# Kernel optimization log

Hardware: AMD Instinct MI355X
Metric: run time of the kernel (lower is better)

Reference implementation:

```python
import jax, jax.numpy as jnp
import numpy as np

N = 100000   # nodes
R = 4        # relations
E = 160000   # edges per relation
DIN = 128
DOUT = 128


def setup_inputs() -> dict:
    key = jax.random.key(0)
    k = jax.random.split(key, 5)
    x = jax.random.normal(k[0], (N, DIN), dtype=jnp.float32)
    src = jax.random.randint(k[1], (R, E), 0, N, dtype=jnp.int32)
    dst = jax.random.randint(k[2], (R, E), 0, N, dtype=jnp.int32)
    # per-relation weights (Linear.weight.T in the original), xavier-ish scale
    W = jax.random.normal(k[3], (R, DIN, DOUT), dtype=jnp.float32) / np.sqrt(DIN)
    Wl = jax.random.normal(k[4], (DIN, DOUT), dtype=jnp.float32) / np.sqrt(DIN)
    b = jnp.zeros((DOUT,), dtype=jnp.float32)
    return {"x": x, "W": W, "Wl": Wl, "b": b, "src": src, "dst": dst}


def reference(x, W, Wl, b, src, dst):
    # DGL GraphConv(norm='right', in==out): aggregate messages first, then matmul.
    def per_rel(s, d):
        agg = jax.ops.segment_sum(x[s], d, num_segments=N)          # [N, DIN]
        deg = jax.ops.segment_sum(jnp.ones(s.shape, x.dtype), d, num_segments=N)
        return agg / jnp.clip(deg, 1.0)[:, None]                     # right norm

    aggs = jax.vmap(per_rel)(src, dst)            # [R, N, DIN]
    h = jnp.einsum('rnd,rde->ne', aggs, W)        # per-relation GEMM + sum over relations
    h = h + x @ Wl + b                            # self-loop Linear with bias
    return jax.nn.relu(h)                         # activation; dropout p=0.0 is identity
```

## Files before the change

### kernel.cpp

```cpp
#include <hip/hip_runtime.h>

#define DIN 128
#define DOUT 128

typedef float f4 __attribute__((ext_vector_type(4)));
typedef float f32x4 __attribute__((ext_vector_type(4)));
typedef short bf16x8 __attribute__((ext_vector_type(8)));
typedef unsigned short u16x8 __attribute__((ext_vector_type(8)));
typedef unsigned short u16x4 __attribute__((ext_vector_type(4)));

__device__ inline unsigned short f2bf(float f) {
    unsigned u = __float_as_uint(f);
    u += 0x7FFFu + ((u >> 16) & 1u);
    return (unsigned short)(u >> 16);
}

__global__ void prep_w(const float* __restrict__ W, const float* __restrict__ Wl,
                       unsigned short* __restrict__ Wt, int total) {
    int id = blockIdx.x * 256 + threadIdx.x;
    if (id >= total) return;
    int m    = id >> 14;
    int rem  = id & 16383;
    int din  = rem >> 7;
    int dout = rem & 127;
    float v = (m < 4) ? W[(m << 14) + din * DOUT + dout] : Wl[din * DOUT + dout];
    Wt[(m << 14) + dout * DIN + din] = f2bf(v);
}

__global__ void prep_x(const float* __restrict__ x, unsigned short* __restrict__ xbf,
                       int total) {
    int tid = blockIdx.x * 256 + threadIdx.x;
    if (tid >= total) return;
    const float* xr = x + (long long)tid * 8;
    f4 lo = *(const f4*)xr;
    f4 hi = *(const f4*)(xr + 4);
    u16x8 p;
    p[0] = f2bf(lo[0]); p[1] = f2bf(lo[1]); p[2] = f2bf(lo[2]); p[3] = f2bf(lo[3]);
    p[4] = f2bf(hi[0]); p[5] = f2bf(hi[1]); p[6] = f2bf(hi[2]); p[7] = f2bf(hi[3]);
    *(u16x8*)&xbf[(long long)tid * 8] = p;
}

__global__ void deg_count(const int* __restrict__ dst, int* __restrict__ cnt,
                          int E, int N, int total) {
    int i = blockIdx.x * 256 + threadIdx.x;
    if (i >= total) return;
    int r = i / E;
    atomicAdd(&cnt[r * N + dst[i]], 1);
}

__global__ void scan1(const int* __restrict__ cnt, int* __restrict__ off,
                      int* __restrict__ part, int M) {
    __shared__ int sd[256];
    const int t = threadIdx.x, b = blockIdx.x;
    const int base = b * 2048 + t * 8;
    int v[8]; int tsum = 0;
    #pragma unroll
    for (int i = 0; i < 8; i++) { int g = base + i; v[i] = (g < M) ? cnt[g] : 0; tsum += v[i]; }
    sd[t] = tsum; __syncthreads();
    for (int d = 1; d < 256; d <<= 1) {
        int val = 0;
        if (t >= d) val = sd[t - d];
        __syncthreads();
        if (t >= d) sd[t] += val;
        __syncthreads();
    }
    int run = sd[t] - tsum;
    if (t == 255) part[b] = sd[255];
    #pragma unroll
    for (int i = 0; i < 8; i++) { int g = base + i; if (g < M) off[g] = run; run += v[i]; }
}

__global__ void scan2(int* __restrict__ part, int nb, int* __restrict__ offM) {
    __shared__ int sd[256];
    const int t = threadIdx.x;
    int v = (t < nb) ? part[t] : 0;
    sd[t] = v; __syncthreads();
    for (int d = 1; d < 256; d <<= 1) {
        int val = 0;
        if (t >= d) val = sd[t - d];
        __syncthreads();
        if (t >= d) sd[t] += val;
        __syncthreads();
    }
    if (t < nb) part[t] = sd[t] - v;
    if (t == 255) *offM = sd[255];
}

__global__ void scan3(int* __restrict__ off, const int* __restrict__ part, int M) {
    const int add = part[blockIdx.x];
    const int base = blockIdx.x * 2048 + threadIdx.x;
    #pragma unroll
    for (int i = 0; i < 8; i++) { int g = base + i * 256; if (g < M) off[g] += add; }
}

__global__ void fill_csr(const int* __restrict__ src, const int* __restrict__ dst,
                         const int* __restrict__ off, int* __restrict__ cnt,
                         int* __restrict__ csr, int E, int N, int total) {
    int i = blockIdx.x * 256 + threadIdx.x;
    if (i >= total) return;
    int r = i / E;
    int idx = r * N + dst[i];
    int pos = atomicAdd(&cnt[idx], -1) - 1;
    csr[off[idx] + pos] = src[i];
}

__global__ __launch_bounds__(256)
void gather_bf(const unsigned short* __restrict__ xbf, const int* __restrict__ off,
               const int* __restrict__ csr, unsigned short* __restrict__ agg,
               int N, int total) {
    int tid = blockIdx.x * 256 + threadIdx.x;
    if (tid >= total) return;
    const int c  = tid & 15;
    const int nn = tid >> 4;
    const int n  = nn % N;
    const int rr = nn / N;

    const int idx = rr * N + n;
    const int s0 = off[idx];
    const int s1 = off[idx + 1];

    float acc[8];
    #pragma unroll
    for (int i = 0; i < 8; i++) acc[i] = 0.0f;

    for (int e = s0; e < s1; e++) {
        const int s = csr[e];
        u16x8 v = *(const u16x8*)&xbf[(long long)s * DIN + c * 8];
        #pragma unroll
        for (int i = 0; i < 8; i++)
            acc[i] += __uint_as_float(((unsigned)v[i]) << 16);
    }
    const float sc = 1.0f / fmaxf((float)(s1 - s0), 1.0f);
    u16x8 p;
    #pragma unroll
    for (int i = 0; i < 8; i++) p[i] = f2bf(acc[i] * sc);
    *(u16x8*)&agg[((long long)rr * N + n) * DIN + c * 8] = p;
}

__global__ __launch_bounds__(256)
void gather_f32(const float* __restrict__ x, const int* __restrict__ off,
                const int* __restrict__ csr, unsigned short* __restrict__ agg,
                int r0, int N, int total) {
    int tid = blockIdx.x * 256 + threadIdx.x;
    if (tid >= total) return;
    const int c  = tid & 31;
    const int nn = tid >> 5;
    const int n  = nn % N;
    const int rr = nn / N;

    const int idx = (r0 + rr) * N + n;
    const int s0 = off[idx];
    const int s1 = off[idx + 1];

    f4 acc = (f4)(0.0f);
    for (int e = s0; e < s1; e++) {
        const int s = csr[e];
        acc += *(const f4*)&x[(long long)s * DIN + c * 4];
    }
    const float sc = 1.0f / fmaxf((float)(s1 - s0), 1.0f);
    acc *= sc;

    u16x4 p;
    p[0] = f2bf(acc[0]); p[1] = f2bf(acc[1]);
    p[2] = f2bf(acc[2]); p[3] = f2bf(acc[3]);
    *(u16x4*)&agg[((long long)rr * N + n) * DIN + c * 4] = p;
}

__global__ __launch_bounds__(256)
void gemm_lds(const float* __restrict__ x, const unsigned short* __restrict__ agg,
              const unsigned short* __restrict__ Wt, const float* __restrict__ bias,
              float* __restrict__ out, int N) {
    __shared__ unsigned short Ws[128 * 128];

    const int t    = threadIdx.x;
    const int lane = t & 63;
    const int w    = t >> 6;
    const int n0   = blockIdx.x * 64;
    const int lr   = lane & 15;
    const int kg   = lane >> 4;
    const int lrm  = lr & 7;

    const int rowA = n0 + w * 16 + lr;
    const int rowC = (rowA < N) ? rowA : (N - 1);

    const long long relStride = (long long)N * DIN;

    f32x4 acc[8];
    #pragma unroll
    for (int ct = 0; ct < 8; ct++) acc[ct] = (f32x4)(0.0f);

    bf16x8 aCur[4], aNxt[4];
    {
        const unsigned short* a0 = agg + (long long)rowC * DIN;
        #pragma unroll
        for (int k = 0; k < 4; k++)
            aCur[k] = *(const bf16x8*)&a0[k * 32 + kg * 8];
    }

    f4 xlo[4], xhi[4];

    for (int r = 0; r < 4; r++) {
        {
            const unsigned short* Wg = Wt + ((long long)r << 14);
            #pragma unroll
            for (int h = 0; h < 2; h++) {
                u16x8 tmp[4];
                #pragma unroll
                for (int p = 0; p < 4; p++) {
                    const int li = t + (h * 4 + p) * 256;
                    tmp[p] = *(const u16x8*)&Wg[((li >> 4) << 7) + (li & 15) * 8];
                }
                #pragma unroll
                for (int p = 0; p < 4; p++) {
                    const int li  = t + (h * 4 + p) * 256;
                    const int row = li >> 4, cg = li & 15;
                    *(u16x8*)&Ws[(row << 7) + ((cg ^ (row & 7)) << 3)] = tmp[p];
                }
            }
        }
        if (r < 3) {
            const unsigned short* an = agg + (r + 1) * relStride + (long long)rowC * DIN;
            #pragma unroll
            for (int k = 0; k < 4; k++)
                aNxt[k] = *(const bf16x8*)&an[k * 32 + kg * 8];
        } else {
            const float* xr = x + (long long)rowC * DIN;
            #pragma unroll
            for (int k = 0; k < 4; k++) {
                xlo[k] = *(const f4*)&xr[k * 32 + kg * 8];
                xhi[k] = *(const f4*)&xr[k * 32 + kg * 8 + 4];
            }
        }
        __syncthreads();

        #pragma unroll
        for (int k0i = 0; k0i < 4; k0i++) {
            #pragma unroll
            for (int ct = 0; ct < 8; ct++) {
                const int row  = ct * 16 + lr;
                const int slot = (k0i * 4 + kg) ^ lrm;
                bf16x8 b = *(const bf16x8*)&Ws[(row << 7) + (slot << 3)];
                acc[ct] = __builtin_amdgcn_mfma_f32_16x16x32_bf16(aCur[k0i], b, acc[ct], 0, 0, 0);
            }
        }
        #pragma unroll
        for (int k = 0; k < 4; k++) aCur[k] = aNxt[k];
        __syncthreads();
    }

    {
        const unsigned short* Wg = Wt + ((long long)4 << 14);
        #pragma unroll
        for (int h = 0; h < 2; h++) {
            u16x8 tmp[4];
            #pragma unroll
            for (int p = 0; p < 4; p++) {
                const int li = t + (h * 4 + p) * 256;
                tmp[p] = *(const u16x8*)&Wg[((li >> 4) << 7) + (li & 15) * 8];
            }
            #pragma unroll
            for (int p = 0; p < 4; p++) {
                const int li  = t + (h * 4 + p) * 256;
                const int row = li >> 4, cg = li & 15;
                *(u16x8*)&Ws[(row << 7) + ((cg ^ (row & 7)) << 3)] = tmp[p];
            }
        }
        __syncthreads();

        #pragma unroll
        for (int k0i = 0; k0i < 4; k0i++) {
            bf16x8 a;
            a[0] = (short)f2bf(xlo[k0i][0]); a[1] = (short)f2bf(xlo[k0i][1]);
            a[2] = (short)f2bf(xlo[k0i][2]); a[3] = (short)f2bf(xlo[k0i][3]);
            a[4] = (short)f2bf(xhi[k0i][0]); a[5] = (short)f2bf(xhi[k0i][1]);
            a[6] = (short)f2bf(xhi[k0i][2]); a[7] = (short)f2bf(xhi[k0i][3]);
            #pragma unroll
            for (int ct = 0; ct < 8; ct++) {
                const int row  = ct * 16 + lr;
                const int slot = (k0i * 4 + kg) ^ lrm;
                bf16x8 b = *(const bf16x8*)&Ws[(row << 7) + (slot << 3)];
                acc[ct] = __builtin_amdgcn_mfma_f32_16x16x32_bf16(a, b, acc[ct], 0, 0, 0);
            }
        }
    }

    #pragma unroll
    for (int j = 0; j < 4; j++) {
        int n2 = n0 + w * 16 + kg * 4 + j;
        if (n2 >= N) continue;
        float* orow = out + (long long)n2 * DOUT + lr;
        #pragma unroll
        for (int ct = 0; ct < 8; ct++) {
            float v = acc[ct][j] + bias[ct * 16 + lr];
            orow[ct * 16] = fmaxf(v, 0.0f);
        }
    }
}

__global__ __launch_bounds__(256, 4)
void gemm_direct(const float* __restrict__ x, const unsigned short* __restrict__ agg,
                 const unsigned short* __restrict__ Wt, const float* __restrict__ bias,
                 float* __restrict__ out, int N, int relStart, int nRel,
                 int doSelf, int accumulate) {
    const int t    = threadIdx.x;
    const int lane = t & 63;
    const int w    = t >> 6;
    const int n0   = blockIdx.x * 64;
    const int lr   = lane & 15;
    const int kg   = lane >> 4;

    const int rowA = n0 + w * 16 + lr;
    const int rowC = (rowA < N) ? rowA : (N - 1);

    f32x4 acc[8];
    #pragma unroll
    for (int ct = 0; ct < 8; ct++) acc[ct] = (f32x4)(0.0f);

    for (int rr = 0; rr < nRel; rr++) {
        const unsigned short* aggR = agg + ((long long)rr * N + rowC) * DIN;
        const unsigned short* WtR  = Wt + ((long long)(relStart + rr) << 14);
        #pragma unroll
        for (int k0 = 0; k0 < DIN; k0 += 32) {
            bf16x8 a = *(const bf16x8*)&aggR[k0 + kg * 8];
            #pragma unroll
            for (int ct = 0; ct < 8; ct++) {
                bf16x8 bfr = *(const bf16x8*)&WtR[((ct * 16 + lr) << 7) + k0 + kg * 8];
                acc[ct] = __builtin_amdgcn_mfma_f32_16x16x32_bf16(a, bfr, acc[ct], 0, 0, 0);
            }
        }
    }

    if (doSelf) {
        const float* xr = x + (long long)rowC * DIN;
        const unsigned short* WtS = Wt + ((long long)4 << 14);
        #pragma unroll
        for (int k0 = 0; k0 < DIN; k0 += 32) {
            f4 v  = *(const f4*)(xr + k0 + kg * 8);
            f4 v2 = *(const f4*)(xr + k0 + kg * 8 + 4);
            bf16x8 a;
            a[0] = (short)f2bf(v[0]);  a[1] = (short)f2bf(v[1]);
            a[2] = (short)f2bf(v[2]);  a[3] = (short)f2bf(v[3]);
            a[4] = (short)f2bf(v2[0]); a[5] = (short)f2bf(v2[1]);
            a[6] = (short)f2bf(v2[2]); a[7] = (short)f2bf(v2[3]);
            #pragma unroll
            for (int ct = 0; ct < 8; ct++) {
                bf16x8 bfr = *(const bf16x8*)&WtS[((ct * 16 + lr) << 7) + k0 + kg * 8];
                acc[ct] = __builtin_amdgcn_mfma_f32_16x16x32_bf16(a, bfr, acc[ct], 0, 0, 0);
            }
        }
    }

    #pragma unroll
    for (int j = 0; j < 4; j++) {
        int n2 = n0 + w * 16 + kg * 4 + j;
        if (n2 >= N) continue;
        float* orow = out + (long long)n2 * DOUT + lr;
        #pragma unroll
        for (int ct = 0; ct < 8; ct++) {
            float v = acc[ct][j];
            if (accumulate) v += orow[ct * 16];
            if (doSelf) {
                v += bias[ct * 16 + lr];
                v = fmaxf(v, 0.0f);
            }
            orow[ct * 16] = v;
        }
    }
}

extern "C" void kernel_launch(void* const* d_in, const int* in_sizes, int n_in,
                              void* d_out, int out_size, void* d_ws, size_t ws_size,
                              hipStream_t stream) {
    const float* x  = (const float*)d_in[0];
    const float* W  = (const float*)d_in[1];
    const float* Wl = (const float*)d_in[2];
    const float* b  = (const float*)d_in[3];
    const int* src  = (const int*)d_in[4];
    const int* dst  = (const int*)d_in[5];
    float* out = (float*)d_out;

    const int N = in_sizes[0] / DIN;
    const int R = in_sizes[1] / (DIN * DOUT);
    const int E = in_sizes[4] / R;
    const int M = R * N;
    const int totE = R * E;

    char* wsp = (char*)d_ws;
    unsigned short* Wt = (unsigned short*)wsp;
    int* cnt  = (int*)(wsp + 5 * 16384 * 2);
    int* off  = cnt + M;
    int* part = off + M + 1;
    int* csr  = part + 256;
    size_t preBytes = ((char*)(csr + totE) - wsp + 255) & ~(size_t)255;
    unsigned short* agg = (unsigned short*)(wsp + preBytes);
    const size_t aggBytes = (size_t)N * DIN * sizeof(unsigned short);
    const bool pathA = (ws_size >= preBytes + 5 * aggBytes) && (R == 4);
    const bool pathB = (ws_size >= preBytes + 4 * aggBytes) && (R == 4);

    hipMemsetAsync(cnt, 0, (size_t)M * sizeof(int), stream);

    prep_w<<<(5 * DIN * DOUT + 255) / 256, 256, 0, stream>>>(W, Wl, Wt, 5 * DIN * DOUT);

    deg_count<<<(totE + 255) / 256, 256, 0, stream>>>(dst, cnt, E, N, totE);

    const int nb = (M + 2047) / 2048;
    scan1<<<nb, 256, 0, stream>>>(cnt, off, part, M);
    scan2<<<1, 256, 0, stream>>>(part, nb, off + M);
    scan3<<<nb, 256, 0, stream>>>(off, part, M);

    fill_csr<<<(totE + 255) / 256, 256, 0, stream>>>(src, dst, off, cnt, csr, E, N, totE);

    const int gemmGrid = (N + 63) / 64;

    if (pathA) {
        unsigned short* xbf = agg + 4 * (size_t)N * DIN;
        prep_x<<<(N * 16 + 255) / 256, 256, 0, stream>>>(x, xbf, N * 16);
        const int total = R * N * 16;
        gather_bf<<<(total + 255) / 256, 256, 0, stream>>>(xbf, off, csr, agg, N, total);
        gemm_lds<<<gemmGrid, 256, 0, stream>>>(x, agg, Wt, b, out, N);
    } else if (pathB) {
        const int total = R * N * 32;
        gather_f32<<<(total + 255) / 256, 256, 0, stream>>>(x, off, csr, agg, 0, N, total);
        gemm_lds<<<gemmGrid, 256, 0, stream>>>(x, agg, Wt, b, out, N);
    } else {
        const int total = N * 32;
        for (int r = 0; r < R; r++) {
            gather_f32<<<(total + 255) / 256, 256, 0, stream>>>(x, off, csr, agg, r, N, total);
            gemm_direct<<<gemmGrid, 256, 0, stream>>>(x, agg, Wt, b, out, N,
                                                      r, 1, (r == R - 1),
                                                      (r > 0));
        }
    }
}
```

Baseline: 187.8 us.

## Fuse prep kernels into one launch and widen GEMM blocks to 128 rows

Merges the weight transpose, x-to-bf16 conversion and degree counting into a single preamble kernel with block-range dispatch, cutting two kernel launches. The GEMM now uses 512-thread blocks covering 128 rows, so each staged weight tile in LDS is reused by twice as many rows, halving weight staging traffic per row. The self-loop term now reads the precomputed bf16 x instead of fp32 x, which folds it into a uniform 5-iteration loop. The larger blocks may lower occupancy, and the fallback path B is removed.

```diff
diff --git a/kernel.cpp b/kernel.cpp
--- a/kernel.cpp
+++ b/kernel.cpp
@@ -15,37 +15,38 @@
     return (unsigned short)(u >> 16);
 }
 
-__global__ void prep_w(const float* __restrict__ W, const float* __restrict__ Wl,
-                       unsigned short* __restrict__ Wt, int total) {
-    int id = blockIdx.x * 256 + threadIdx.x;
-    if (id >= total) return;
-    int m    = id >> 14;
-    int rem  = id & 16383;
-    int din  = rem >> 7;
-    int dout = rem & 127;
-    float v = (m < 4) ? W[(m << 14) + din * DOUT + dout] : Wl[din * DOUT + dout];
-    Wt[(m << 14) + dout * DIN + din] = f2bf(v);
-}
-
-__global__ void prep_x(const float* __restrict__ x, unsigned short* __restrict__ xbf,
-                       int total) {
-    int tid = blockIdx.x * 256 + threadIdx.x;
-    if (tid >= total) return;
-    const float* xr = x + (long long)tid * 8;
-    f4 lo = *(const f4*)xr;
-    f4 hi = *(const f4*)(xr + 4);
-    u16x8 p;
-    p[0] = f2bf(lo[0]); p[1] = f2bf(lo[1]); p[2] = f2bf(lo[2]); p[3] = f2bf(lo[3]);
-    p[4] = f2bf(hi[0]); p[5] = f2bf(hi[1]); p[6] = f2bf(hi[2]); p[7] = f2bf(hi[3]);
-    *(u16x8*)&xbf[(long long)tid * 8] = p;
-}
-
-__global__ void deg_count(const int* __restrict__ dst, int* __restrict__ cnt,
-                          int E, int N, int total) {
-    int i = blockIdx.x * 256 + threadIdx.x;
-    if (i >= total) return;
-    int r = i / E;
-    atomicAdd(&cnt[r * N + dst[i]], 1);
+__global__ void preamble(const float* __restrict__ W, const float* __restrict__ Wl,
+                         const float* __restrict__ x, const int* __restrict__ dst,
+                         unsigned short* __restrict__ Wt, unsigned short* __restrict__ xbf,
+                         int* __restrict__ cnt,
+                         int nbW, int nbX, int E, int N, int totE) {
+    const int b = blockIdx.x;
+    const int t = threadIdx.x;
+    if (b < nbW) {
+        int id = b * 256 + t;
+        if (id >= 5 * DIN * DOUT) return;
+        int m    = id >> 14;
+        int rem  = id & 16383;
+        int din  = rem >> 7;
+        int dout = rem & 127;
+        float v = (m < 4) ? W[(m << 14) + din * DOUT + dout] : Wl[din * DOUT + dout];
+        Wt[(m << 14) + dout * DIN + din] = f2bf(v);
+    } else if (b < nbW + nbX) {
+        int tid = (b - nbW) * 256 + t;
+        if (tid >= N * 16) return;
+        const float* xr = x + (long long)tid * 8;
+        f4 lo = *(const f4*)xr;
+        f4 hi = *(const f4*)(xr + 4);
+        u16x8 p;
+        p[0] = f2bf(lo[0]); p[1] = f2bf(lo[1]); p[2] = f2bf(lo[2]); p[3] = f2bf(lo[3]);
+        p[4] = f2bf(hi[0]); p[5] = f2bf(hi[1]); p[6] = f2bf(hi[2]); p[7] = f2bf(hi[3]);
+        *(u16x8*)&xbf[(long long)tid * 8] = p;
+    } else {
+        int i = (b - nbW - nbX) * 256 + t;
+        if (i >= totE) return;
+        int r = i / E;
+        atomicAdd(&cnt[r * N + dst[i]], 1);
+    }
 }
 
 __global__ void scan1(const int* __restrict__ cnt, int* __restrict__ off,
@@ -166,16 +167,18 @@
     *(u16x4*)&agg[((long long)rr * N + n) * DIN + c * 4] = p;
 }
 
-__global__ __launch_bounds__(256)
-void gemm_lds(const float* __restrict__ x, const unsigned short* __restrict__ agg,
-              const unsigned short* __restrict__ Wt, const float* __restrict__ bias,
+__global__ __launch_bounds__(512, 2)
+void gemm_lds(const unsigned short* __restrict__ agg,
+              const unsigned short* __restrict__ xbf,
+              const unsigned short* __restrict__ Wt,
+              const float* __restrict__ bias,
               float* __restrict__ out, int N) {
     __shared__ unsigned short Ws[128 * 128];
 
     const int t    = threadIdx.x;
     const int lane = t & 63;
     const int w    = t >> 6;
-    const int n0   = blockIdx.x * 64;
+    const int n0   = blockIdx.x * 128;
     const int lr   = lane & 15;
     const int kg   = lane >> 4;
     const int lrm  = lr & 7;
@@ -189,47 +192,36 @@
     #pragma unroll
     for (int ct = 0; ct < 8; ct++) acc[ct] = (f32x4)(0.0f);
 
+    const unsigned short* aSrc0 = agg + (long long)rowC * DIN;
+
     bf16x8 aCur[4], aNxt[4];
-    {
-        const unsigned short* a0 = agg + (long long)rowC * DIN;
-        #pragma unroll
-        for (int k = 0; k < 4; k++)
-            aCur[k] = *(const bf16x8*)&a0[k * 32 + kg * 8];
-    }
-
-    f4 xlo[4], xhi[4];
-
-    for (int r = 0; r < 4; r++) {
+    #pragma unroll
+    for (int k = 0; k < 4; k++)
+        aCur[k] = *(const bf16x8*)&aSrc0[k * 32 + kg * 8];
+
+    for (int r = 0; r < 5; r++) {
         {
             const unsigned short* Wg = Wt + ((long long)r << 14);
-            #pragma unroll
-            for (int h = 0; h < 2; h++) {
-                u16x8 tmp[4];
-                #pragma unroll
-                for (int p = 0; p < 4; p++) {
-                    const int li = t + (h * 4 + p) * 256;
-                    tmp[p] = *(const u16x8*)&Wg[((li >> 4) << 7) + (li & 15) * 8];
-                }
-                #pragma unroll
-                for (int p = 0; p < 4; p++) {
-                    const int li  = t + (h * 4 + p) * 256;
-                    const int row = li >> 4, cg = li & 15;
-                    *(u16x8*)&Ws[(row << 7) + ((cg ^ (row & 7)) << 3)] = tmp[p];
-                }
-            }
-        }
-        if (r < 3) {
-            const unsigned short* an = agg + (r + 1) * relStride + (long long)rowC * DIN;
+            u16x8 tmp[4];
+            #pragma unroll
+            for (int p = 0; p < 4; p++) {
+                const int li = t + p * 512;
+                tmp[p] = *(const u16x8*)&Wg[((li >> 4) << 7) + (li & 15) * 8];
+            }
+            #pragma unroll
+            for (int p = 0; p < 4; p++) {
+                const int li  = t + p * 512;
+                const int row = li >> 4, cg = li & 15;
+                *(u16x8*)&Ws[(row << 7) + ((cg ^ (row & 7)) << 3)] = tmp[p];
+            }
+        }
+        if (r < 4) {
+            const unsigned short* an = (r < 3)
+                ? agg + (r + 1) * relStride + (long long)rowC * DIN
+                : xbf + (long long)rowC * DIN;
             #pragma unroll
             for (int k = 0; k < 4; k++)
                 aNxt[k] = *(const bf16x8*)&an[k * 32 + kg * 8];
-        } else {
-            const float* xr = x + (long long)rowC * DIN;
-            #pragma unroll
-            for (int k = 0; k < 4; k++) {
-                xlo[k] = *(const f4*)&xr[k * 32 + kg * 8];
-                xhi[k] = *(const f4*)&xr[k * 32 + kg * 8 + 4];
-            }
         }
         __syncthreads();
 
@@ -243,44 +235,10 @@
                 acc[ct] = __builtin_amdgcn_mfma_f32_16x16x32_bf16(aCur[k0i], b, acc[ct], 0, 0, 0);
             }
         }
-        #pragma unroll
-        for (int k = 0; k < 4; k++) aCur[k] = aNxt[k];
-        __syncthreads();
-    }
-
-    {
-        const unsigned short* Wg = Wt + ((long long)4 << 14);
-        #pragma unroll
-        for (int h = 0; h < 2; h++) {
-            u16x8 tmp[4];
-            #pragma unroll
-            for (int p = 0; p < 4; p++) {
-                const int li = t + (h * 4 + p) * 256;
-                tmp[p] = *(const u16x8*)&Wg[((li >> 4) << 7) + (li & 15) * 8];
-            }
-            #pragma unroll
-            for (int p = 0; p < 4; p++) {
-                const int li  = t + (h * 4 + p) * 256;
-                const int row = li >> 4, cg = li & 15;
-                *(u16x8*)&Ws[(row << 7) + ((cg ^ (row & 7)) << 3)] = tmp[p];
-            }
-        }
-        __syncthreads();
-
-        #pragma unroll
-        for (int k0i = 0; k0i < 4; k0i++) {
-            bf16x8 a;
-            a[0] = (short)f2bf(xlo[k0i][0]); a[1] = (short)f2bf(xlo[k0i][1]);
-            a[2] = (short)f2bf(xlo[k0i][2]); a[3] = (short)f2bf(xlo[k0i][3]);
-            a[4] = (short)f2bf(xhi[k0i][0]); a[5] = (short)f2bf(xhi[k0i][1]);
-            a[6] = (short)f2bf(xhi[k0i][2]); a[7] = (short)f2bf(xhi[k0i][3]);
-            #pragma unroll
-            for (int ct = 0; ct < 8; ct++) {
-                const int row  = ct * 16 + lr;
-                const int slot = (k0i * 4 + kg) ^ lrm;
-                bf16x8 b = *(const bf16x8*)&Ws[(row << 7) + (slot << 3)];
-                acc[ct] = __builtin_amdgcn_mfma_f32_16x16x32_bf16(a, b, acc[ct], 0, 0, 0);
-            }
+        if (r < 4) {
+            #pragma unroll
+            for (int k = 0; k < 4; k++) aCur[k] = aNxt[k];
+            __syncthreads();
         }
     }
 
@@ -395,35 +353,41 @@
     unsigned short* agg = (unsigned short*)(wsp + preBytes);
     const size_t aggBytes = (size_t)N * DIN * sizeof(unsigned short);
     const bool pathA = (ws_size >= preBytes + 5 * aggBytes) && (R == 4);
-    const bool pathB = (ws_size >= preBytes + 4 * aggBytes) && (R == 4);
 
     hipMemsetAsync(cnt, 0, (size_t)M * sizeof(int), stream);
 
-    prep_w<<<(5 * DIN * DOUT + 255) / 256, 256, 0, stream>>>(W, Wl, Wt, 5 * DIN * DOUT);
-
-    deg_count<<<(totE + 255) / 256, 256, 0, stream>>>(dst, cnt, E, N, totE);
-
     const int nb = (M + 2047) / 2048;
-    scan1<<<nb, 256, 0, stream>>>(cnt, off, part, M);
-    scan2<<<1, 256, 0, stream>>>(part, nb, off + M);
-    scan3<<<nb, 256, 0, stream>>>(off, part, M);
-
-    fill_csr<<<(totE + 255) / 256, 256, 0, stream>>>(src, dst, off, cnt, csr, E, N, totE);
-
-    const int gemmGrid = (N + 63) / 64;
 
     if (pathA) {
         unsigned short* xbf = agg + 4 * (size_t)N * DIN;
-        prep_x<<<(N * 16 + 255) / 256, 256, 0, stream>>>(x, xbf, N * 16);
+
+        const int nbW = (5 * DIN * DOUT + 255) / 256;
+        const int nbX = (N * 16 + 255) / 256;
+        const int nbD = (totE + 255) / 256;
+        preamble<<<nbW + nbX + nbD, 256, 0, stream>>>(W, Wl, x, dst, Wt, xbf, cnt,
+                                                      nbW, nbX, E, N, totE);
+
+        scan1<<<nb, 256, 0, stream>>>(cnt, off, part, M);
+        scan2<<<1, 256, 0, stream>>>(part, nb, off + M);
+        scan3<<<nb, 256, 0, stream>>>(off, part, M);
+        fill_csr<<<(totE + 255) / 256, 256, 0, stream>>>(src, dst, off, cnt, csr, E, N, totE);
+
         const int total = R * N * 16;
         gather_bf<<<(total + 255) / 256, 256, 0, stream>>>(xbf, off, csr, agg, N, total);
-        gemm_lds<<<gemmGrid, 256, 0, stream>>>(x, agg, Wt, b, out, N);
-    } else if (pathB) {
-        const int total = R * N * 32;
-        gather_f32<<<(total + 255) / 256, 256, 0, stream>>>(x, off, csr, agg, 0, N, total);
-        gemm_lds<<<gemmGrid, 256, 0, stream>>>(x, agg, Wt, b, out, N);
+
+        gemm_lds<<<(N + 127) / 128, 512, 0, stream>>>(agg, xbf, Wt, b, out, N);
     } else {
+        const int nbW = (5 * DIN * DOUT + 255) / 256;
+        const int nbD = (totE + 255) / 256;
+        preamble<<<nbW + nbD, 256, 0, stream>>>(W, Wl, x, dst, Wt, nullptr, cnt,
+                                                nbW, 0, E, N, totE);
+        scan1<<<nb, 256, 0, stream>>>(cnt, off, part, M);
+        scan2<<<1, 256, 0, stream>>>(part, nb, off + M);
+        scan3<<<nb, 256, 0, stream>>>(off, part, M);
+        fill_csr<<<(totE + 255) / 256, 256, 0, stream>>>(src, dst, off, cnt, csr, E, N, totE);
+
         const int total = N * 32;
+        const int gemmGrid = (N + 63) / 64;
         for (int r = 0; r < R; r++) {
             gather_f32<<<(total + 255) / 256, 256, 0, stream>>>(x, off, csr, agg, r, N, total);
             gemm_direct<<<gemmGrid, 256, 0, stream>>>(x, agg, Wt, b, out, N,
```

Result: faster. 174.6 us, median of 2 (-7.1%).
